# Performance work log

Hardware: AMD Instinct MI355X
Metric: run time of the kernel (lower is better)

Reference implementation:

```python
import jax, jax.numpy as jnp
import numpy as np

V = 1_000_000   # variables
F = 4_200_000   # functions (clauses), ratio ~4.2
K = 3           # literals per clause
E = K * F       # edges
T = 5           # fixed number of peel iterations (peel update is idempotent once converged)


def setup_inputs() -> dict:
    key = jax.random.key(0)
    k1, k2 = jax.random.split(key, 2)
    vidx = jax.random.randint(k1, (E,), 0, V, dtype=jnp.int32)
    fidx = jnp.repeat(jnp.arange(F, dtype=jnp.int32), K)  # each clause touches K variables
    graph_map = jnp.stack([vidx, fidx])  # [2, E]
    edge_feature = (2 * jax.random.randint(k2, (E,), 0, 2) - 1).astype(jnp.float32)  # +/-1 literal signs
    active_variables = jnp.ones((V, 1), jnp.float32)
    active_functions = jnp.ones((F, 1), jnp.float32)
    return dict(graph_map=graph_map, edge_feature=edge_feature,
                active_variables=active_variables, active_functions=active_functions)


def reference(graph_map, edge_feature, active_variables, active_functions):
    """Peeling propagation over the bipartite variable-function graph.

    Equivalent to the torch sparse-mm formulation:
      vf_map @ x        == segment_sum(x[fidx], vidx, V)
      signed_vf_map @ x == segment_sum(edge_feature * x[fidx], vidx, V)
      vf_map^T @ y      == segment_sum(y[vidx], fidx, F)
    """
    nV = active_variables.shape[0]
    nF = active_functions.shape[0]
    vidx = graph_map[0]
    fidx = graph_map[1]
    ef = edge_feature[:, None]  # [E,1]

    def seg_v(x_f):        # vf_map @ x_f : [F,1] -> [V,1]
        return jax.ops.segment_sum(x_f[fidx], vidx, num_segments=nV)

    def seg_v_signed(x_f):  # signed_vf_map @ x_f
        return jax.ops.segment_sum(ef * x_f[fidx], vidx, num_segments=nV)

    def seg_f(x_v):        # vf_map^T @ x_v : [V,1] -> [F,1]
        return jax.ops.segment_sum(x_v[vidx], fidx, num_segments=nF)

    variable_degree = seg_v(active_functions)
    signed_variable_degree = seg_v_signed(active_functions)

    def step(carry, _):
        av, af, deg, sdeg = carry
        # variables whose active clause occurrences all share one sign
        single_v = (deg == jnp.abs(sdeg)).astype(deg.dtype) * av
        # active clauses touched by those variables become satisfied
        single_f = (seg_f(single_v) > 0).astype(af.dtype) * af
        deg = deg - seg_v(single_f) * av
        sdeg = sdeg - seg_v_signed(single_f) * av
        av = av * (1.0 - single_v)
        af = af * (1.0 - single_f)
        return (av, af, deg, sdeg), None

    (av, af, deg, sdeg), _ = jax.lax.scan(
        step, (active_variables, active_functions, variable_degree, signed_variable_degree),
        None, length=T)
    return deg  # residual variable degrees after peeling [V,1]
```

## Files before the change

### kernel.cpp

```cpp
#include <hip/hip_runtime.h>


static constexpr int Vn = 1000000;
static constexpr int Fn = 4200000;
static constexpr int Tn = 5;

static constexpr int SBLK = 2048;
static constexpr int FPB  = 2052;
static constexpr int BIN_BITS = 10;
static constexpr int BIN_SIZE = 1 << BIN_BITS;
static constexpr int NB  = (Vn + BIN_SIZE - 1) >> BIN_BITS;
static constexpr int NBP = 1024;
static constexpr int CH_BITS = 12;
static constexpr int CH_SIZE = 1 << CH_BITS;
static constexpr int NCH = (Vn + CH_SIZE - 1) >> CH_BITS;
static constexpr int RCAP = 3 * FPB;
static constexpr int RSTRIDE = (RCAP + 63) & ~63;
static constexpr int OROW = 1024;
static constexpr int AVW = NCH * (CH_SIZE / 64);

__global__ __launch_bounds__(256) void k_pack_sort(
    const int* __restrict__ vidx, const float* __restrict__ ef,
    const float* __restrict__ afunc,
    unsigned long long* __restrict__ gpack,
    unsigned short* __restrict__ offs,
    unsigned short* __restrict__ sorted)
{
    __shared__ unsigned int cur[NBP];
    __shared__ unsigned int wsum[4];
    __shared__ unsigned int s_total;
    __shared__ __align__(16) unsigned short st[RSTRIDE];

    const int k = blockIdx.x;
    const int f0 = k * FPB;
    int n = Fn - f0; if (n < 0) n = 0; if (n > FPB) n = FPB;
    const int n4 = n >> 2;

    for (int i = threadIdx.x; i < NBP; i += 256) cur[i] = 0u;
    __syncthreads();

    for (int j = threadIdx.x; j < n4; j += 256) {
        const int fb = f0 + 4 * j, e = 3 * fb;
        int4 va = *(const int4*)(vidx + e);
        int4 vb = *(const int4*)(vidx + e + 4);
        int4 vc = *(const int4*)(vidx + e + 8);
        float4 ea = *(const float4*)(ef + e);
        float4 eb = *(const float4*)(ef + e + 4);
        float4 ec = *(const float4*)(ef + e + 8);
        float4 a4 = *(const float4*)(afunc + fb);
        int      vv[12] = {va.x, va.y, va.z, va.w, vb.x, vb.y, vb.z, vb.w, vc.x, vc.y, vc.z, vc.w};
        float    ss[12] = {ea.x, ea.y, ea.z, ea.w, eb.x, eb.y, eb.z, eb.w, ec.x, ec.y, ec.z, ec.w};
        float    aa[4]  = {a4.x, a4.y, a4.z, a4.w};
        unsigned long long gq[4];
        #pragma unroll
        for (int q = 0; q < 4; ++q) {
            int v0 = vv[3 * q], v1 = vv[3 * q + 1], v2 = vv[3 * q + 2];
            unsigned int s0 = ss[3 * q]     > 0.0f ? 1u : 0u;
            unsigned int s1 = ss[3 * q + 1] > 0.0f ? 1u : 0u;
            unsigned int s2 = ss[3 * q + 2] > 0.0f ? 1u : 0u;
            unsigned int act = aa[q] != 0.0f ? 1u : 0u;
            gq[q] = (unsigned long long)(unsigned int)v0
                  | ((unsigned long long)(unsigned int)v1 << 20)
                  | ((unsigned long long)(unsigned int)v2 << 40)
                  | ((unsigned long long)s0 << 60)
                  | ((unsigned long long)s1 << 61)
                  | ((unsigned long long)s2 << 62)
                  | ((unsigned long long)act << 63);
            if (act) {
                atomicAdd(&cur[v0 >> BIN_BITS], 1u);
                atomicAdd(&cur[v1 >> BIN_BITS], 1u);
                atomicAdd(&cur[v2 >> BIN_BITS], 1u);
            }
        }
        *(ulonglong2*)(gpack + fb)     = make_ulonglong2(gq[0], gq[1]);
        *(ulonglong2*)(gpack + fb + 2) = make_ulonglong2(gq[2], gq[3]);
    }
    __syncthreads();

    {
        const int t = threadIdx.x, lane = t & 63, wid = t >> 6;
        unsigned int a0 = cur[4 * t], a1 = cur[4 * t + 1];
        unsigned int a2 = cur[4 * t + 2], a3 = cur[4 * t + 3];
        unsigned int tsum = a0 + a1 + a2 + a3;
        unsigned int x = tsum;
        #pragma unroll
        for (int off = 1; off < 64; off <<= 1) {
            unsigned int y = (unsigned int)__shfl_up((int)x, off);
            if (lane >= off) x += y;
        }
        if (lane == 63) wsum[wid] = x;
        __syncthreads();
        unsigned int wbase = 0;
        for (int w = 0; w < wid; ++w) wbase += wsum[w];
        unsigned int e0x = wbase + x - tsum;
        unsigned int e1x = e0x + a0, e2x = e1x + a1, e3x = e2x + a2;
        cur[4 * t] = e0x; cur[4 * t + 1] = e1x; cur[4 * t + 2] = e2x; cur[4 * t + 3] = e3x;
        if (t == 255) s_total = e3x + a3;
        unsigned short* row = offs + (size_t)k * OROW;
        if (4 * t     <= NB) row[4 * t]     = (unsigned short)e0x;
        if (4 * t + 1 <= NB) row[4 * t + 1] = (unsigned short)e1x;
        if (4 * t + 2 <= NB) row[4 * t + 2] = (unsigned short)e2x;
        if (4 * t + 3 <= NB) row[4 * t + 3] = (unsigned short)e3x;
    }
    __syncthreads();

    for (int j = threadIdx.x; j < n4; j += 256) {
        const int fb = f0 + 4 * j;
        ulonglong2 ga = *(const ulonglong2*)(gpack + fb);
        ulonglong2 gb = *(const ulonglong2*)(gpack + fb + 2);
        unsigned long long gq[4] = {ga.x, ga.y, gb.x, gb.y};
        #pragma unroll
        for (int q = 0; q < 4; ++q) {
            unsigned long long g = gq[q];
            if ((long long)g < 0) {
                unsigned int v0 = (unsigned int)(g & 0xFFFFFu);
                unsigned int v1 = (unsigned int)((g >> 20) & 0xFFFFFu);
                unsigned int v2 = (unsigned int)((g >> 40) & 0xFFFFFu);
                unsigned int sl0 = atomicAdd(&cur[v0 >> BIN_BITS], 1u);
                st[sl0] = (unsigned short)((v0 & (CH_SIZE - 1)) | ((unsigned int)((g >> 60) & 1u) << CH_BITS));
                unsigned int sl1 = atomicAdd(&cur[v1 >> BIN_BITS], 1u);
                st[sl1] = (unsigned short)((v1 & (CH_SIZE - 1)) | ((unsigned int)((g >> 61) & 1u) << CH_BITS));
                unsigned int sl2 = atomicAdd(&cur[v2 >> BIN_BITS], 1u);
                st[sl2] = (unsigned short)((v2 & (CH_SIZE - 1)) | ((unsigned int)((g >> 62) & 1u) << CH_BITS));
            }
        }
    }
    __syncthreads();

    {
        const int tot = (int)s_total;
        const int nvec = (tot + 7) >> 3;
        int4* __restrict__ dst = (int4*)(sorted + (size_t)k * RSTRIDE);
        const int4* __restrict__ src = (const int4*)st;
        for (int i = threadIdx.x; i < nvec; i += 256) dst[i] = src[i];
    }
}

__device__ __forceinline__ unsigned char subdirty8(unsigned long long m) {
    unsigned char b = 0;
    #pragma unroll
    for (int j = 0; j < 8; ++j) b |= (unsigned char)((((m >> (8 * j)) & 0xFFull) ? 1u : 0u) << j);
    return b;
}

__global__ __launch_bounds__(1024) void k_accum(
    const unsigned short* __restrict__ offs,
    const unsigned short* __restrict__ sorted,
    const float* __restrict__ avars,
    unsigned int* __restrict__ packed,
    unsigned long long* __restrict__ avm,
    unsigned long long* __restrict__ svm,
    unsigned char* __restrict__ sgrp8,
    unsigned int* __restrict__ tmp,
    unsigned char* __restrict__ tgrp)
{
    __shared__ unsigned int acc[CH_SIZE];
    __shared__ unsigned short row0[SBLK];
    __shared__ unsigned short row1[SBLK];
    const int c = blockIdx.x;
    const int r0 = 4 * c;
    const int r1 = (4 * c + 4 < NB) ? (4 * c + 4) : NB;
    for (int i = threadIdx.x; i < CH_SIZE; i += 1024) acc[i] = 0u;
    for (int i = threadIdx.x; i < SBLK; i += 1024) {
        row0[i] = offs[(size_t)i * OROW + r0];
        row1[i] = offs[(size_t)i * OROW + r1];
    }
    __syncthreads();
    for (int k = threadIdx.x; k < SBLK; k += 1024) {
        const int s0 = row0[k], s1 = row1[k];
        const unsigned short* seg = sorted + (size_t)k * RSTRIDE;
        int e = s0;
        for (; e < s1 && (e & 3); ++e) {
            unsigned int p = seg[e];
            atomicAdd(&acc[p & (CH_SIZE - 1)], 0x10000u | (p >> CH_BITS));
        }
        for (; e + 4 <= s1; e += 4) {
            unsigned long long q = *(const unsigned long long*)(seg + e);
            #pragma unroll
            for (int j = 0; j < 4; ++j) {
                unsigned int p = (unsigned int)((q >> (16 * j)) & 0xFFFFu);
                atomicAdd(&acc[p & (CH_SIZE - 1)], 0x10000u | (p >> CH_BITS));
            }
        }
        for (; e < s1; ++e) {
            unsigned int p = seg[e];
            atomicAdd(&acc[p & (CH_SIZE - 1)], 0x10000u | (p >> CH_BITS));
        }
    }
    __syncthreads();
    const int vbase = c << CH_BITS;
    for (int i = threadIdx.x; i < CH_SIZE; i += 1024) {
        int v = vbase + i;
        bool valid = v < Vn;
        unsigned int p = valid ? acc[i] : 0u;
        bool av = valid && (avars[v] != 0.0f);
        unsigned int cnt = p >> 16, pos = p & 0xFFFFu;
        bool sv = av && (pos == 0u || pos == cnt);
        unsigned long long avb = __ballot(av);
        unsigned long long svb = __ballot(sv);
        if (valid) { packed[v] = p; tmp[v] = 0u; }
        if ((threadIdx.x & 63) == 0) {
            avm[v >> 6] = avb;
            svm[v >> 6] = svb;
            sgrp8[v >> 6] = subdirty8(svb);
            tgrp[v >> 6] = 0;
        }
    }
}

__device__ __forceinline__ void fire_one(unsigned long long g, int f,
                                         unsigned long long* __restrict__ gpack,
                                         const unsigned int* __restrict__ svm32,
                                         const unsigned char* __restrict__ s8,
                                         unsigned int* __restrict__ tmp,
                                         unsigned char* __restrict__ tgrp)
{
    if ((long long)g >= 0) return;
    unsigned int v0 = (unsigned int)(g & 0xFFFFFu);
    unsigned int v1 = (unsigned int)((g >> 20) & 0xFFFFFu);
    unsigned int v2 = (unsigned int)((g >> 40) & 0xFFFFFu);
    unsigned int h0 = (unsigned int)(s8[v0 >> 6] >> ((v0 >> 3) & 7u)) & 1u;
    unsigned int h1 = (unsigned int)(s8[v1 >> 6] >> ((v1 >> 3) & 7u)) & 1u;
    unsigned int h2 = (unsigned int)(s8[v2 >> 6] >> ((v2 >> 3) & 7u)) & 1u;
    if (!(h0 | h1 | h2)) return;
    unsigned int hit = ((svm32[v0 >> 5] >> (v0 & 31u)) |
                        (svm32[v1 >> 5] >> (v1 & 31u)) |
                        (svm32[v2 >> 5] >> (v2 & 31u))) & 1u;
    if (!hit) return;
    gpack[f] = g & ~(1ull << 63);
    atomicAdd(&tmp[v0], 0x10000u | (unsigned int)((g >> 60) & 1u));
    atomicAdd(&tmp[v1], 0x10000u | (unsigned int)((g >> 61) & 1u));
    atomicAdd(&tmp[v2], 0x10000u | (unsigned int)((g >> 62) & 1u));
    tgrp[v0 >> 6] = 1; tgrp[v1 >> 6] = 1; tgrp[v2 >> 6] = 1;
}

static constexpr int FBLOCKS = 1024;

__global__ __launch_bounds__(256) void k_funcs(unsigned long long* __restrict__ gpack,
                        const unsigned int* __restrict__ svm32,
                        const unsigned char* __restrict__ sgrp8,
                        unsigned int* __restrict__ tmp,
                        unsigned char* __restrict__ tgrp)
{
    __shared__ __align__(16) unsigned char s8[AVW];
    for (int i = threadIdx.x; i < AVW / 16; i += 256)
        ((int4*)s8)[i] = ((const int4*)sgrp8)[i];
    __syncthreads();
    const int step = FBLOCKS * 256 * 8;
    for (int f = (blockIdx.x * 256 + threadIdx.x) * 8; f < Fn; f += step) {
        ulonglong2 ga = *(const ulonglong2*)(gpack + f);
        ulonglong2 gb = *(const ulonglong2*)(gpack + f + 2);
        ulonglong2 gc = *(const ulonglong2*)(gpack + f + 4);
        ulonglong2 gd = *(const ulonglong2*)(gpack + f + 6);
        fire_one(ga.x, f,     gpack, svm32, s8, tmp, tgrp);
        fire_one(ga.y, f + 1, gpack, svm32, s8, tmp, tgrp);
        fire_one(gb.x, f + 2, gpack, svm32, s8, tmp, tgrp);
        fire_one(gb.y, f + 3, gpack, svm32, s8, tmp, tgrp);
        fire_one(gc.x, f + 4, gpack, svm32, s8, tmp, tgrp);
        fire_one(gc.y, f + 5, gpack, svm32, s8, tmp, tgrp);
        fire_one(gd.x, f + 6, gpack, svm32, s8, tmp, tgrp);
        fire_one(gd.y, f + 7, gpack, svm32, s8, tmp, tgrp);
    }
}

__global__ void k_update(unsigned int* __restrict__ packed,
                         unsigned int* __restrict__ tmp,
                         unsigned long long* __restrict__ avm,
                         unsigned long long* __restrict__ svm,
                         unsigned char* __restrict__ sgrp8,
                         unsigned char* __restrict__ tgrp,
                         float* __restrict__ deg, int write_deg)
{
    const int v = blockIdx.x * blockDim.x + threadIdx.x;
    const int lane = threadIdx.x & 63;
    const bool valid = v < Vn;
    unsigned long long avw = 0ull, svw = 0ull;
    unsigned char tg = 0;
    if (valid) {
        avw = avm[v >> 6]; svw = svm[v >> 6];
        tg = tgrp[v >> 6];
    }
    if (!write_deg && !tg && svw == 0ull) return;
    const bool av_old = valid && ((avw >> lane) & 1ull);
    const bool sv     = valid && ((svw >> lane) & 1ull);
    const bool av_new = av_old && !sv;
    unsigned int p = 0u;
    if (valid) {
        p = packed[v];
        if (tg) {
            unsigned int tp = tmp[v];
            if (tp != 0u) {
                if (av_old) { p -= tp; packed[v] = p; }
                tmp[v] = 0u;
            }
        }
    }
    const unsigned int c = p >> 16, pos = p & 0xFFFFu;
    const bool nsv = av_new && (pos == 0u || pos == c);
    unsigned long long nsvb = __ballot(nsv);
    if (lane == 0 && valid) {
        svm[v >> 6] = nsvb;
        avm[v >> 6] = avw & ~svw;
        sgrp8[v >> 6] = subdirty8(nsvb);
        if (tg) tgrp[v >> 6] = 0;
    }
    if (write_deg && valid) deg[v] = (float)c;
}

extern "C" void kernel_launch(void* const* d_in, const int* in_sizes, int n_in,
                              void* d_out, int out_size, void* d_ws, size_t ws_size,
                              hipStream_t stream) {
    const int*   graph_map        = (const int*)d_in[0];
    const float* edge_feature     = (const float*)d_in[1];
    const float* active_variables = (const float*)d_in[2];
    const float* active_functions = (const float*)d_in[3];
    const int* vidx = graph_map;

    float* deg = (float*)d_out;
    char* ws = (char*)d_ws;
    size_t off = 0;
    auto alloc = [&](size_t bytes) -> void* {
        void* p = ws + off; off += (bytes + 255) & ~(size_t)255; return p;
    };
    unsigned long long* gpack = (unsigned long long*)alloc(8ull * Fn);
    unsigned int* packed      = (unsigned int*)alloc(4ull * Vn);
    unsigned long long* avm   = (unsigned long long*)alloc(8ull * AVW);
    unsigned long long* svm   = (unsigned long long*)alloc(8ull * AVW);
    unsigned char* sgrp8      = (unsigned char*)alloc(AVW);
    unsigned char* tgrp       = (unsigned char*)alloc(AVW);
    unsigned short* offs      = (unsigned short*)alloc(2ull * SBLK * OROW);
    unsigned short* sorted    = (unsigned short*)alloc(2ull * SBLK * RSTRIDE);
    unsigned int* tmp         = (unsigned int*)alloc(4ull * Vn);

    const int BS = 256;
    const int gV = (Vn + BS - 1) / BS;

    k_pack_sort<<<SBLK, 256, 0, stream>>>(vidx, edge_feature, active_functions,
                                          gpack, offs, sorted);
    k_accum<<<NCH, 1024, 0, stream>>>(offs, sorted, active_variables, packed,
                                      avm, svm, sgrp8, tmp, tgrp);
    for (int t = 0; t < Tn; ++t) {
        k_funcs<<<FBLOCKS, BS, 0, stream>>>(gpack, (const unsigned int*)svm, sgrp8, tmp, tgrp);
        k_update<<<gV, BS, 0, stream>>>(packed, tmp, avm, svm, sgrp8, tgrp, deg, (t == Tn - 1) ? 1 : 0);
    }
}
```

Before: 305.1 us.

## Keep packed clauses in registers for scatter pass and refine dirty-group granularity

The pack-sort kernel now holds each thread's (at most three) packed clause groups in registers between the histogram and scatter passes, instead of re-reading them from the global gpack buffer. Separately, the per-64-variable summary of single-sign variables goes from 8 bits (groups of 8 variables) to 16 bits (groups of 4 variables). The finer summary lets k_funcs skip more clauses before the global svm gather. The cost is more register use in pack-sort, twice the shared-memory footprint for the summary in k_funcs, and a fixed three-iteration unroll that assumes FPB/4 <= 768.

```diff
diff --git a/kernel.cpp b/kernel.cpp
--- a/kernel.cpp
+++ b/kernel.cpp
@@ -35,50 +35,61 @@
     const int f0 = k * FPB;
     int n = Fn - f0; if (n < 0) n = 0; if (n > FPB) n = FPB;
     const int n4 = n >> 2;
-
-    for (int i = threadIdx.x; i < NBP; i += 256) cur[i] = 0u;
-    __syncthreads();
-
-    for (int j = threadIdx.x; j < n4; j += 256) {
-        const int fb = f0 + 4 * j, e = 3 * fb;
-        int4 va = *(const int4*)(vidx + e);
-        int4 vb = *(const int4*)(vidx + e + 4);
-        int4 vc = *(const int4*)(vidx + e + 8);
-        float4 ea = *(const float4*)(ef + e);
-        float4 eb = *(const float4*)(ef + e + 4);
-        float4 ec = *(const float4*)(ef + e + 8);
-        float4 a4 = *(const float4*)(afunc + fb);
-        int      vv[12] = {va.x, va.y, va.z, va.w, vb.x, vb.y, vb.z, vb.w, vc.x, vc.y, vc.z, vc.w};
-        float    ss[12] = {ea.x, ea.y, ea.z, ea.w, eb.x, eb.y, eb.z, eb.w, ec.x, ec.y, ec.z, ec.w};
-        float    aa[4]  = {a4.x, a4.y, a4.z, a4.w};
-        unsigned long long gq[4];
-        #pragma unroll
-        for (int q = 0; q < 4; ++q) {
-            int v0 = vv[3 * q], v1 = vv[3 * q + 1], v2 = vv[3 * q + 2];
-            unsigned int s0 = ss[3 * q]     > 0.0f ? 1u : 0u;
-            unsigned int s1 = ss[3 * q + 1] > 0.0f ? 1u : 0u;
-            unsigned int s2 = ss[3 * q + 2] > 0.0f ? 1u : 0u;
-            unsigned int act = aa[q] != 0.0f ? 1u : 0u;
-            gq[q] = (unsigned long long)(unsigned int)v0
-                  | ((unsigned long long)(unsigned int)v1 << 20)
-                  | ((unsigned long long)(unsigned int)v2 << 40)
-                  | ((unsigned long long)s0 << 60)
-                  | ((unsigned long long)s1 << 61)
-                  | ((unsigned long long)s2 << 62)
-                  | ((unsigned long long)act << 63);
-            if (act) {
-                atomicAdd(&cur[v0 >> BIN_BITS], 1u);
-                atomicAdd(&cur[v1 >> BIN_BITS], 1u);
-                atomicAdd(&cur[v2 >> BIN_BITS], 1u);
-            }
-        }
-        *(ulonglong2*)(gpack + fb)     = make_ulonglong2(gq[0], gq[1]);
-        *(ulonglong2*)(gpack + fb + 2) = make_ulonglong2(gq[2], gq[3]);
-    }
+    const int t = threadIdx.x;
+
+    for (int i = t; i < NBP; i += 256) cur[i] = 0u;
+    __syncthreads();
+
+    const int j0 = t, j1 = t + 256, j2 = t + 512;
+    const bool has0 = j0 < n4, has1 = j1 < n4, has2 = j2 < n4;
+    unsigned long long q0a=0,q0b=0,q0c=0,q0d=0, q1a=0,q1b=0,q1c=0,q1d=0, q2a=0,q2b=0,q2c=0,q2d=0;
+
+#define PROC(J, QA, QB, QC, QD) do {                                               \
+    const int fb = f0 + 4 * (J), e = 3 * fb;                                       \
+    int4 va = *(const int4*)(vidx + e);                                            \
+    int4 vb = *(const int4*)(vidx + e + 4);                                        \
+    int4 vc = *(const int4*)(vidx + e + 8);                                        \
+    float4 ea = *(const float4*)(ef + e);                                          \
+    float4 eb = *(const float4*)(ef + e + 4);                                      \
+    float4 ec = *(const float4*)(ef + e + 8);                                      \
+    float4 a4 = *(const float4*)(afunc + fb);                                      \
+    int   vv[12] = {va.x,va.y,va.z,va.w,vb.x,vb.y,vb.z,vb.w,vc.x,vc.y,vc.z,vc.w};  \
+    float ss[12] = {ea.x,ea.y,ea.z,ea.w,eb.x,eb.y,eb.z,eb.w,ec.x,ec.y,ec.z,ec.w};  \
+    float aa[4]  = {a4.x,a4.y,a4.z,a4.w};                                          \
+    unsigned long long gq[4];                                                      \
+    _Pragma("unroll")                                                              \
+    for (int q = 0; q < 4; ++q) {                                                  \
+        int v0 = vv[3*q], v1 = vv[3*q+1], v2 = vv[3*q+2];                          \
+        unsigned int s0 = ss[3*q]   > 0.0f ? 1u : 0u;                              \
+        unsigned int s1 = ss[3*q+1] > 0.0f ? 1u : 0u;                              \
+        unsigned int s2 = ss[3*q+2] > 0.0f ? 1u : 0u;                              \
+        unsigned int act = aa[q] != 0.0f ? 1u : 0u;                                \
+        gq[q] = (unsigned long long)(unsigned int)v0                               \
+              | ((unsigned long long)(unsigned int)v1 << 20)                       \
+              | ((unsigned long long)(unsigned int)v2 << 40)                       \
+              | ((unsigned long long)s0 << 60)                                     \
+              | ((unsigned long long)s1 << 61)                                     \
+              | ((unsigned long long)s2 << 62)                                     \
+              | ((unsigned long long)act << 63);                                   \
+        if (act) {                                                                 \
+            atomicAdd(&cur[v0 >> BIN_BITS], 1u);                                   \
+            atomicAdd(&cur[v1 >> BIN_BITS], 1u);                                   \
+            atomicAdd(&cur[v2 >> BIN_BITS], 1u);                                   \
+        }                                                                          \
+    }                                                                              \
+    *(ulonglong2*)(gpack + fb)     = make_ulonglong2(gq[0], gq[1]);                \
+    *(ulonglong2*)(gpack + fb + 2) = make_ulonglong2(gq[2], gq[3]);                \
+    QA = gq[0]; QB = gq[1]; QC = gq[2]; QD = gq[3];                                \
+} while (0)
+
+    if (has0) PROC(j0, q0a, q0b, q0c, q0d);
+    if (has1) PROC(j1, q1a, q1b, q1c, q1d);
+    if (has2) PROC(j2, q2a, q2b, q2c, q2d);
+#undef PROC
     __syncthreads();
 
     {
-        const int t = threadIdx.x, lane = t & 63, wid = t >> 6;
+        const int lane = t & 63, wid = t >> 6;
         unsigned int a0 = cur[4 * t], a1 = cur[4 * t + 1];
         unsigned int a2 = cur[4 * t + 2], a3 = cur[4 * t + 3];
         unsigned int tsum = a0 + a1 + a2 + a3;
@@ -104,27 +115,24 @@
     }
     __syncthreads();
 
-    for (int j = threadIdx.x; j < n4; j += 256) {
-        const int fb = f0 + 4 * j;
-        ulonglong2 ga = *(const ulonglong2*)(gpack + fb);
-        ulonglong2 gb = *(const ulonglong2*)(gpack + fb + 2);
-        unsigned long long gq[4] = {ga.x, ga.y, gb.x, gb.y};
-        #pragma unroll
-        for (int q = 0; q < 4; ++q) {
-            unsigned long long g = gq[q];
-            if ((long long)g < 0) {
-                unsigned int v0 = (unsigned int)(g & 0xFFFFFu);
-                unsigned int v1 = (unsigned int)((g >> 20) & 0xFFFFFu);
-                unsigned int v2 = (unsigned int)((g >> 40) & 0xFFFFFu);
-                unsigned int sl0 = atomicAdd(&cur[v0 >> BIN_BITS], 1u);
-                st[sl0] = (unsigned short)((v0 & (CH_SIZE - 1)) | ((unsigned int)((g >> 60) & 1u) << CH_BITS));
-                unsigned int sl1 = atomicAdd(&cur[v1 >> BIN_BITS], 1u);
-                st[sl1] = (unsigned short)((v1 & (CH_SIZE - 1)) | ((unsigned int)((g >> 61) & 1u) << CH_BITS));
-                unsigned int sl2 = atomicAdd(&cur[v2 >> BIN_BITS], 1u);
-                st[sl2] = (unsigned short)((v2 & (CH_SIZE - 1)) | ((unsigned int)((g >> 62) & 1u) << CH_BITS));
-            }
-        }
-    }
+#define SCAT1(G, SBIT) do {                                                        \
+    unsigned long long g = (G);                                                    \
+    if ((long long)g < 0) {                                                        \
+        unsigned int v0 = (unsigned int)(g & 0xFFFFFu);                            \
+        unsigned int v1 = (unsigned int)((g >> 20) & 0xFFFFFu);                    \
+        unsigned int v2 = (unsigned int)((g >> 40) & 0xFFFFFu);                    \
+        unsigned int sl0 = atomicAdd(&cur[v0 >> BIN_BITS], 1u);                    \
+        st[sl0] = (unsigned short)((v0 & (CH_SIZE-1)) | ((unsigned int)((g >> 60) & 1u) << CH_BITS)); \
+        unsigned int sl1 = atomicAdd(&cur[v1 >> BIN_BITS], 1u);                    \
+        st[sl1] = (unsigned short)((v1 & (CH_SIZE-1)) | ((unsigned int)((g >> 61) & 1u) << CH_BITS)); \
+        unsigned int sl2 = atomicAdd(&cur[v2 >> BIN_BITS], 1u);                    \
+        st[sl2] = (unsigned short)((v2 & (CH_SIZE-1)) | ((unsigned int)((g >> 62) & 1u) << CH_BITS)); \
+    }                                                                              \
+} while (0)
+    if (has0) { SCAT1(q0a, 0); SCAT1(q0b, 0); SCAT1(q0c, 0); SCAT1(q0d, 0); }
+    if (has1) { SCAT1(q1a, 0); SCAT1(q1b, 0); SCAT1(q1c, 0); SCAT1(q1d, 0); }
+    if (has2) { SCAT1(q2a, 0); SCAT1(q2b, 0); SCAT1(q2c, 0); SCAT1(q2d, 0); }
+#undef SCAT1
     __syncthreads();
 
     {
@@ -132,15 +140,16 @@
         const int nvec = (tot + 7) >> 3;
         int4* __restrict__ dst = (int4*)(sorted + (size_t)k * RSTRIDE);
         const int4* __restrict__ src = (const int4*)st;
-        for (int i = threadIdx.x; i < nvec; i += 256) dst[i] = src[i];
-    }
-}
-
-__device__ __forceinline__ unsigned char subdirty8(unsigned long long m) {
-    unsigned char b = 0;
+        for (int i = t; i < nvec; i += 256) dst[i] = src[i];
+    }
+}
+
+__device__ __forceinline__ unsigned short subdirty4(unsigned long long m) {
+    unsigned int r = 0;
     #pragma unroll
-    for (int j = 0; j < 8; ++j) b |= (unsigned char)((((m >> (8 * j)) & 0xFFull) ? 1u : 0u) << j);
-    return b;
+    for (int j = 0; j < 16; ++j)
+        r |= (((m >> (4 * j)) & 0xFull) ? 1u : 0u) << j;
+    return (unsigned short)r;
 }
 
 __global__ __launch_bounds__(1024) void k_accum(
@@ -150,7 +159,7 @@
     unsigned int* __restrict__ packed,
     unsigned long long* __restrict__ avm,
     unsigned long long* __restrict__ svm,
-    unsigned char* __restrict__ sgrp8,
+    unsigned short* __restrict__ sgrp4,
     unsigned int* __restrict__ tmp,
     unsigned char* __restrict__ tgrp)
 {
@@ -202,7 +211,7 @@
         if ((threadIdx.x & 63) == 0) {
             avm[v >> 6] = avb;
             svm[v >> 6] = svb;
-            sgrp8[v >> 6] = subdirty8(svb);
+            sgrp4[v >> 6] = subdirty4(svb);
             tgrp[v >> 6] = 0;
         }
     }
@@ -211,7 +220,7 @@
 __device__ __forceinline__ void fire_one(unsigned long long g, int f,
                                          unsigned long long* __restrict__ gpack,
                                          const unsigned int* __restrict__ svm32,
-                                         const unsigned char* __restrict__ s8,
+                                         const unsigned short* __restrict__ s4,
                                          unsigned int* __restrict__ tmp,
                                          unsigned char* __restrict__ tgrp)
 {
@@ -219,9 +228,9 @@
     unsigned int v0 = (unsigned int)(g & 0xFFFFFu);
     unsigned int v1 = (unsigned int)((g >> 20) & 0xFFFFFu);
     unsigned int v2 = (unsigned int)((g >> 40) & 0xFFFFFu);
-    unsigned int h0 = (unsigned int)(s8[v0 >> 6] >> ((v0 >> 3) & 7u)) & 1u;
-    unsigned int h1 = (unsigned int)(s8[v1 >> 6] >> ((v1 >> 3) & 7u)) & 1u;
-    unsigned int h2 = (unsigned int)(s8[v2 >> 6] >> ((v2 >> 3) & 7u)) & 1u;
+    unsigned int h0 = (unsigned int)(s4[v0 >> 6] >> ((v0 >> 2) & 15u)) & 1u;
+    unsigned int h1 = (unsigned int)(s4[v1 >> 6] >> ((v1 >> 2) & 15u)) & 1u;
+    unsigned int h2 = (unsigned int)(s4[v2 >> 6] >> ((v2 >> 2) & 15u)) & 1u;
     if (!(h0 | h1 | h2)) return;
     unsigned int hit = ((svm32[v0 >> 5] >> (v0 & 31u)) |
                         (svm32[v1 >> 5] >> (v1 & 31u)) |
@@ -238,13 +247,13 @@
 
 __global__ __launch_bounds__(256) void k_funcs(unsigned long long* __restrict__ gpack,
                         const unsigned int* __restrict__ svm32,
-                        const unsigned char* __restrict__ sgrp8,
+                        const unsigned short* __restrict__ sgrp4,
                         unsigned int* __restrict__ tmp,
                         unsigned char* __restrict__ tgrp)
 {
-    __shared__ __align__(16) unsigned char s8[AVW];
-    for (int i = threadIdx.x; i < AVW / 16; i += 256)
-        ((int4*)s8)[i] = ((const int4*)sgrp8)[i];
+    __shared__ __align__(16) unsigned short s4[AVW];
+    for (int i = threadIdx.x; i < AVW / 8; i += 256)
+        ((int4*)s4)[i] = ((const int4*)sgrp4)[i];
     __syncthreads();
     const int step = FBLOCKS * 256 * 8;
     for (int f = (blockIdx.x * 256 + threadIdx.x) * 8; f < Fn; f += step) {
@@ -252,14 +261,14 @@
         ulonglong2 gb = *(const ulonglong2*)(gpack + f + 2);
         ulonglong2 gc = *(const ulonglong2*)(gpack + f + 4);
         ulonglong2 gd = *(const ulonglong2*)(gpack + f + 6);
-        fire_one(ga.x, f,     gpack, svm32, s8, tmp, tgrp);
-        fire_one(ga.y, f + 1, gpack, svm32, s8, tmp, tgrp);
-        fire_one(gb.x, f + 2, gpack, svm32, s8, tmp, tgrp);
-        fire_one(gb.y, f + 3, gpack, svm32, s8, tmp, tgrp);
-        fire_one(gc.x, f + 4, gpack, svm32, s8, tmp, tgrp);
-        fire_one(gc.y, f + 5, gpack, svm32, s8, tmp, tgrp);
-        fire_one(gd.x, f + 6, gpack, svm32, s8, tmp, tgrp);
-        fire_one(gd.y, f + 7, gpack, svm32, s8, tmp, tgrp);
+        fire_one(ga.x, f,     gpack, svm32, s4, tmp, tgrp);
+        fire_one(ga.y, f + 1, gpack, svm32, s4, tmp, tgrp);
+        fire_one(gb.x, f + 2, gpack, svm32, s4, tmp, tgrp);
+        fire_one(gb.y, f + 3, gpack, svm32, s4, tmp, tgrp);
+        fire_one(gc.x, f + 4, gpack, svm32, s4, tmp, tgrp);
+        fire_one(gc.y, f + 5, gpack, svm32, s4, tmp, tgrp);
+        fire_one(gd.x, f + 6, gpack, svm32, s4, tmp, tgrp);
+        fire_one(gd.y, f + 7, gpack, svm32, s4, tmp, tgrp);
     }
 }
 
@@ -267,7 +276,7 @@
                          unsigned int* __restrict__ tmp,
                          unsigned long long* __restrict__ avm,
                          unsigned long long* __restrict__ svm,
-                         unsigned char* __restrict__ sgrp8,
+                         unsigned short* __restrict__ sgrp4,
                          unsigned char* __restrict__ tgrp,
                          float* __restrict__ deg, int write_deg)
 {
@@ -301,7 +310,7 @@
     if (lane == 0 && valid) {
         svm[v >> 6] = nsvb;
         avm[v >> 6] = avw & ~svw;
-        sgrp8[v >> 6] = subdirty8(nsvb);
+        sgrp4[v >> 6] = subdirty4(nsvb);
         if (tg) tgrp[v >> 6] = 0;
     }
     if (write_deg && valid) deg[v] = (float)c;
@@ -326,7 +335,7 @@
     unsigned int* packed      = (unsigned int*)alloc(4ull * Vn);
     unsigned long long* avm   = (unsigned long long*)alloc(8ull * AVW);
     unsigned long long* svm   = (unsigned long long*)alloc(8ull * AVW);
-    unsigned char* sgrp8      = (unsigned char*)alloc(AVW);
+    unsigned short* sgrp4     = (unsigned short*)alloc(2ull * AVW);
     unsigned char* tgrp       = (unsigned char*)alloc(AVW);
     unsigned short* offs      = (unsigned short*)alloc(2ull * SBLK * OROW);
     unsigned short* sorted    = (unsigned short*)alloc(2ull * SBLK * RSTRIDE);
@@ -338,9 +347,9 @@
     k_pack_sort<<<SBLK, 256, 0, stream>>>(vidx, edge_feature, active_functions,
                                           gpack, offs, sorted);
     k_accum<<<NCH, 1024, 0, stream>>>(offs, sorted, active_variables, packed,
-                                      avm, svm, sgrp8, tmp, tgrp);
+                                      avm, svm, sgrp4, tmp, tgrp);
     for (int t = 0; t < Tn; ++t) {
-        k_funcs<<<FBLOCKS, BS, 0, stream>>>(gpack, (const unsigned int*)svm, sgrp8, tmp, tgrp);
-        k_update<<<gV, BS, 0, stream>>>(packed, tmp, avm, svm, sgrp8, tgrp, deg, (t == Tn - 1) ? 1 : 0);
-    }
-}
+        k_funcs<<<FBLOCKS, BS, 0, stream>>>(gpack, (const unsigned int*)svm, sgrp4, tmp, tgrp);
+        k_update<<<gV, BS, 0, stream>>>(packed, tmp, avm, svm, sgrp4, tgrp, deg, (t == Tn - 1) ? 1 : 0);
+    }
+}
```

Result: no change. 306.4 us (+0.4%).
